# Kernel optimization log

Hardware: AMD Instinct MI355X
Metric: run time of the kernel (lower is better)

Reference implementation:

```python
import jax, jax.numpy as jnp
import numpy as np

S, B, D, H, A = 256, 1024, 64, 128, 8  # seq_len, buffer, state_size, hidden, action_size


def _init(key, shape, fan_in):
    bound = 1.0 / np.sqrt(fan_in)
    return jax.random.uniform(key, shape, jnp.float32, -bound, bound)


def setup_inputs() -> dict:
    key = jax.random.key(0)
    ks = jax.random.split(key, 24)
    inp = {"state": jax.random.normal(ks[0], (S, B, D), jnp.float32)}
    # actor / critic MLPs (Linear(D,H) + ReLU + Linear(H,H) + ReLU)
    inp["aw1"] = _init(ks[1], (H, D), D); inp["ab1"] = _init(ks[2], (H,), D)
    inp["aw2"] = _init(ks[3], (H, H), H); inp["ab2"] = _init(ks[4], (H,), H)
    inp["cw1"] = _init(ks[5], (H, D), D); inp["cb1"] = _init(ks[6], (H,), D)
    inp["cw2"] = _init(ks[7], (H, H), H); inp["cb2"] = _init(ks[8], (H,), H)
    # LSTMs (PyTorch layout: W_ih [4H,H], W_hh [4H,H], gate order i,f,g,o)
    inp["a_wih"] = _init(ks[9], (4 * H, H), H); inp["a_whh"] = _init(ks[10], (4 * H, H), H)
    inp["a_bih"] = _init(ks[11], (4 * H,), H); inp["a_bhh"] = _init(ks[12], (4 * H,), H)
    inp["c_wih"] = _init(ks[13], (4 * H, H), H); inp["c_whh"] = _init(ks[14], (4 * H, H), H)
    inp["c_bih"] = _init(ks[15], (4 * H,), H); inp["c_bhh"] = _init(ks[16], (4 * H,), H)
    # heads
    inp["mw"] = _init(ks[17], (A, H), H); inp["mb"] = _init(ks[18], (A,), H)
    inp["lw"] = _init(ks[19], (A, H), H); inp["lb"] = _init(ks[20], (A,), H)
    inp["vw"] = _init(ks[21], (1, H), H); inp["vb"] = _init(ks[22], (1,), H)
    return inp


def _mlp(x, w1, b1, w2, b2):
    h = jax.nn.relu(jnp.einsum('sbd,hd->sbh', x, w1) + b1)
    return jax.nn.relu(jnp.einsum('sbh,gh->sbg', h, w2) + b2)


def _lstm_zero_state(x, w_ih, b_ih, b_hh):
    # Each timestep runs with fresh zero (h, c): the recurrent term vanishes,
    # so the whole sequence is one batched GEMM + gating (W_hh unused).
    gates = jnp.einsum('sbh,gh->sbg', x, w_ih) + b_ih + b_hh  # [S,B,4H]
    i, f, g, o = jnp.split(gates, 4, axis=-1)
    c = jax.nn.sigmoid(i) * jnp.tanh(g)  # f * c_prev = 0
    return jax.nn.sigmoid(o) * jnp.tanh(c)


def reference(state, aw1, ab1, aw2, ab2, cw1, cb1, cw2, cb2,
              a_wih, a_whh, a_bih, a_bhh, c_wih, c_whh, c_bih, c_bhh,
              mw, mb, lw, lb, vw, vb):
    actor_h = _lstm_zero_state(_mlp(state, aw1, ab1, aw2, ab2), a_wih, a_bih, a_bhh)
    critic_h = _lstm_zero_state(_mlp(state, cw1, cb1, cw2, cb2), c_wih, c_bih, c_bhh)
    mean = jnp.einsum('sbh,ah->sba', actor_h, mw) + mb
    std = jnp.exp(jnp.einsum('sbh,ah->sba', actor_h, lw) + lb)
    value = jnp.einsum('sbh,vh->sbv', critic_h, vw) + vb
    return (mean, std, value)
```

## Files before the change

### kernel.cpp

```cpp
#include <hip/hip_runtime.h>


#define NROWS (256 * 1024)
#define HID 128
#define ACTD 8

#define W1_OFF 0
#define W2_OFF 16384
#define WI_OFF 49152
#define WG_OFF 81920
#define WO_OFF 114688
#define PSTR 147456
#define HEAD_OFF (2 * PSTR)
#define GB_OFF (HEAD_OFF + 8192)

#define NEG_L (-1.4426950408889634f)
#define TWO_L (2.8853900817779268f)

typedef __attribute__((ext_vector_type(8))) short s16x8;
typedef __attribute__((ext_vector_type(4))) float fx4;
typedef __attribute__((ext_vector_type(2))) float fx2;
typedef __attribute__((ext_vector_type(2))) unsigned int u32x2;
typedef __attribute__((ext_vector_type(4))) unsigned int u32x4;

__device__ __forceinline__ unsigned int cvtpk(float lo, float hi) {
  unsigned int r;
  asm("v_cvt_pk_bf16_f32 %0, %1, %2" : "=v"(r) : "v"(lo), "v"(hi));
  return r;
}
__device__ __forceinline__ float ex2(float x) {
  return __builtin_amdgcn_exp2f(x);
}
__device__ __forceinline__ float frcp(float x) {
  return __builtin_amdgcn_rcpf(x);
}
__device__ __forceinline__ fx2 mk2(float a, float b) {
  fx2 v;
  v[0] = a;
  v[1] = b;
  return v;
}

__device__ __forceinline__ s16x8 frag_ld(const unsigned short* base, int row,
                                         int kbyte, int rowsh) {
  int byte = (row << rowsh) + (kbyte ^ ((row & 7) << 4));
  return *(const s16x8*)((const char*)base + byte);
}

struct wpair {
  s16x8 w0, w1;
};
template <int KC>
__device__ __forceinline__ wpair wload(const char* __restrict__ wimg, int wv,
                                       int kc, int woff) {
  wpair p;
  p.w0 = *(const s16x8*)(wimg + (((wv * 2 + 0) * KC + kc) << 10) + woff);
  p.w1 = *(const s16x8*)(wimg + (((wv * 2 + 1) * KC + kc) << 10) + woff);
  return p;
}

template <int ASH>
__device__ __forceinline__ void gemm_kc(const wpair& p,
                                        const unsigned short* at, int kbyte,
                                        int l15, fx4 acc[4][2]) {
#pragma unroll
  for (int jt = 0; jt < 4; ++jt) {
    s16x8 a = frag_ld(at, jt * 16 + l15, kbyte, ASH);
    acc[jt][0] = __builtin_amdgcn_mfma_f32_16x16x32_bf16(p.w0, a, acc[jt][0], 0, 0, 0);
    acc[jt][1] = __builtin_amdgcn_mfma_f32_16x16x32_bf16(p.w1, a, acc[jt][1], 0, 0, 0);
  }
}

__device__ __forceinline__ void zacc(fx4 acc[4][2]) {
#pragma unroll
  for (int j = 0; j < 4; ++j)
#pragma unroll
    for (int i = 0; i < 2; ++i) acc[j][i] = fx4{0.f, 0.f, 0.f, 0.f};
}
__device__ __forceinline__ void bacc(fx4 acc[4][2], const float* __restrict__ b,
                                     int fb, int g4) {
#pragma unroll
  for (int it = 0; it < 2; ++it) {
    fx4 bv = *(const fx4*)(b + fb + it * 16 + g4);
#pragma unroll
    for (int jt = 0; jt < 4; ++jt) acc[jt][it] = bv;
  }
}

__device__ __forceinline__ void epi_relu(fx4 acc[4][2], unsigned short* obuf,
                                         int fb, int lane) {
  const int g4 = (lane >> 4) << 2;
  const int l15 = lane & 15;
  char* ob = (char*)obuf;
#pragma unroll
  for (int it = 0; it < 2; ++it) {
    int n0 = fb + it * 16 + g4;
#pragma unroll
    for (int jt = 0; jt < 4; ++jt) {
      fx4 v = acc[jt][it];
#pragma unroll
      for (int r = 0; r < 4; ++r) v[r] = fmaxf(v[r], 0.0f);
      u32x2 u;
      u[0] = cvtpk(v[0], v[1]);
      u[1] = cvtpk(v[2], v[3]);
      int m = jt * 16 + l15;
      *(u32x2*)(ob + (m << 8) + ((n0 * 2) ^ ((m & 7) << 4))) = u;
    }
  }
}

__global__ void prep_weights(const float* __restrict__ aw1,
                             const float* __restrict__ aw2,
                             const float* __restrict__ awih,
                             const float* __restrict__ cw1,
                             const float* __restrict__ cw2,
                             const float* __restrict__ cwih,
                             const float* __restrict__ mw,
                             const float* __restrict__ lw,
                             const float* __restrict__ vw,
                             const float* __restrict__ abih,
                             const float* __restrict__ abhh,
                             const float* __restrict__ cbih,
                             const float* __restrict__ cbhh,
                             char* __restrict__ ws) {
  int y = blockIdx.y;
  int idx = blockIdx.x * 256 + threadIdx.x;
  if (y >= 12) {
    if (idx < 384) {
      float* dst = (float*)(ws + GB_OFF + (size_t)(y - 12) * 1536);
      const float* b0 = (y == 12) ? abih : cbih;
      const float* b1 = (y == 12) ? abhh : cbhh;
      int sect = idx >> 7, f = idx & 127;
      int srow = (sect == 0) ? f : (sect == 1) ? 256 + f : 384 + f;
      float scale = (sect == 1) ? TWO_L : NEG_L;
      dst[idx] = scale * (b0[srow] + b1[srow]);
    }
    return;
  }
  if (y >= 10) {
    if (idx >= 256) return;
    int row = idx >> 4, c16 = idx & 15, kc = c16 >> 2, ks = c16 & 3;
    fx4 v0 = {0.f, 0.f, 0.f, 0.f}, v1 = v0;
    if (y == 10) {
      const float* src = (row < 8) ? (mw + (size_t)row * HID + c16 * 8)
                                   : (lw + (size_t)(row - 8) * HID + c16 * 8);
      v0 = ((const fx4*)src)[0];
      v1 = ((const fx4*)src)[1];
    } else if (row == 0) {
      const float* src = vw + c16 * 8;
      v0 = ((const fx4*)src)[0];
      v1 = ((const fx4*)src)[1];
    }
    u32x4 u;
    u[0] = cvtpk(v0[0], v0[1]);
    u[1] = cvtpk(v0[2], v0[3]);
    u[2] = cvtpk(v1[0], v1[1]);
    u[3] = cvtpk(v1[2], v1[3]);
    int dst = ((kc * 4 + ks) * 16 + row) * 16;
    *(u32x4*)(ws + HEAD_OFF + (size_t)(y - 10) * 4096 + dst) = u;
    return;
  }
  const float* src;
  int nch, ksh, KC, off;
  switch (y) {
    case 0:  src = aw1;              nch = 1024; ksh = 3; KC = 2; off = W1_OFF;        break;
    case 1:  src = aw2;              nch = 2048; ksh = 4; KC = 4; off = W2_OFF;        break;
    case 2:  src = awih;             nch = 2048; ksh = 4; KC = 4; off = WI_OFF;        break;
    case 3:  src = awih + 256 * HID; nch = 2048; ksh = 4; KC = 4; off = WG_OFF;        break;
    case 4:  src = awih + 384 * HID; nch = 2048; ksh = 4; KC = 4; off = WO_OFF;        break;
    case 5:  src = cw1;              nch = 1024; ksh = 3; KC = 2; off = PSTR + W1_OFF; break;
    case 6:  src = cw2;              nch = 2048; ksh = 4; KC = 4; off = PSTR + W2_OFF; break;
    case 7:  src = cwih;             nch = 2048; ksh = 4; KC = 4; off = PSTR + WI_OFF; break;
    case 8:  src = cwih + 256 * HID; nch = 2048; ksh = 4; KC = 4; off = PSTR + WG_OFF; break;
    default: src = cwih + 384 * HID; nch = 2048; ksh = 4; KC = 4; off = PSTR + WO_OFF; break;
  }
  if (idx >= nch) return;
  int row = idx >> ksh;
  int c16 = idx & ((1 << ksh) - 1);
  int b2 = row >> 4, r = row & 15, kc = c16 >> 2, ks = c16 & 3;
  const fx4* gp = (const fx4*)(src + (size_t)idx * 8);
  fx4 v0 = gp[0], v1 = gp[1];
  u32x4 u;
  u[0] = cvtpk(v0[0], v0[1]);
  u[1] = cvtpk(v0[2], v0[3]);
  u[2] = cvtpk(v1[0], v1[1]);
  u[3] = cvtpk(v1[2], v1[3]);
  int dst = (((b2 * KC + kc) * 4 + ks) * 16 + r) * 16;
  *(u32x4*)(ws + off + dst) = u;
}

__global__ __launch_bounds__(256, 3) void fused_ac(
    const float* __restrict__ state, const float* __restrict__ ab1,
    const float* __restrict__ ab2, const float* __restrict__ cb1,
    const float* __restrict__ cb2, const float* __restrict__ mb,
    const float* __restrict__ lb, const float* __restrict__ vb,
    const char* __restrict__ ws, float* __restrict__ outp) {
  __shared__ __align__(16) unsigned short abuf[8192];
  __shared__ __align__(16) unsigned short hbuf[8192];

  const int tid = threadIdx.x;
  const int lane = tid & 63;
  const int wv = tid >> 6;
  const int l15 = lane & 15;
  const int g4 = (lane >> 4) << 2;
  const int kb0 = (lane >> 4) << 4;
  const int woff = ((lane >> 4) << 8) + (l15 << 4);
  const int fb = wv << 5;
  const int path = blockIdx.x >> 12;
  const int rbase = (blockIdx.x & 4095) << 6;

  const char* wsp = ws + (size_t)path * PSTR;
  const float* b1 = path ? cb1 : ab1;
  const float* b2 = path ? cb2 : ab2;
  const float* gb = (const float*)(ws + GB_OFF + (size_t)path * 1536);
  const char* himg = ws + HEAD_OFF + (size_t)path * 4096;

  float* meanp = outp;
  float* stdp = outp + (size_t)NROWS * ACTD;
  float* valp = outp + (size_t)NROWS * ACTD * 2;

  wpair w1a = wload<2>(wsp + W1_OFF, wv, 0, woff);
  wpair w1b = wload<2>(wsp + W1_OFF, wv, 1, woff);

  {
    const float* xg = state + (size_t)rbase * 64;
    char* ab = (char*)abuf;
#pragma unroll
    for (int i = 0; i < 2; ++i) {
      int idx = tid + i * 256;
      int r = idx >> 3, c = idx & 7;
      const fx4* gp = (const fx4*)(xg + idx * 8);
      fx4 v0 = gp[0], v1 = gp[1];
      u32x4 u;
      u[0] = cvtpk(v0[0], v0[1]);
      u[1] = cvtpk(v0[2], v0[3]);
      u[2] = cvtpk(v1[0], v1[1]);
      u[3] = cvtpk(v1[2], v1[3]);
      *(u32x4*)(ab + r * 128 + ((c << 4) ^ ((r & 7) << 4))) = u;
    }
  }
  __syncthreads();

  fx4 acc[4][2];
  bacc(acc, b1, fb, g4);
  __builtin_amdgcn_s_setprio(1);
  gemm_kc<7>(w1a, abuf, 0 + kb0, l15, acc);
  gemm_kc<7>(w1b, abuf, 64 + kb0, l15, acc);
  __builtin_amdgcn_s_setprio(0);
  wpair w2a = wload<4>(wsp + W2_OFF, wv, 0, woff);
  wpair w2b = wload<4>(wsp + W2_OFF, wv, 1, woff);
  epi_relu(acc, hbuf, fb, lane);
  __syncthreads();

  bacc(acc, b2, fb, g4);
  __builtin_amdgcn_s_setprio(1);
  gemm_kc<8>(w2a, hbuf, 0 + kb0, l15, acc);
  gemm_kc<8>(w2b, hbuf, 64 + kb0, l15, acc);
  {
    wpair p = wload<4>(wsp + W2_OFF, wv, 2, woff);
    gemm_kc<8>(p, hbuf, 128 + kb0, l15, acc);
  }
  {
    wpair p = wload<4>(wsp + W2_OFF, wv, 3, woff);
    gemm_kc<8>(p, hbuf, 192 + kb0, l15, acc);
  }
  __builtin_amdgcn_s_setprio(0);
  wpair pi0 = wload<4>(wsp + WI_OFF, wv, 0, woff);
  wpair pg0 = wload<4>(wsp + WG_OFF, wv, 0, woff);
  wpair po0 = wload<4>(wsp + WO_OFF, wv, 0, woff);
  epi_relu(acc, abuf, fb, lane);
  __syncthreads();

  fx4 ai[4][2], ag[4][2], ao[4][2];
  zacc(ai);
  zacc(ag);
  zacc(ao);
  __builtin_amdgcn_s_setprio(1);
#pragma unroll
  for (int kc = 0; kc < 4; ++kc) {
    wpair pi = (kc == 0) ? pi0 : wload<4>(wsp + WI_OFF, wv, kc, woff);
    wpair pg = (kc == 0) ? pg0 : wload<4>(wsp + WG_OFF, wv, kc, woff);
    wpair po = (kc == 0) ? po0 : wload<4>(wsp + WO_OFF, wv, kc, woff);
    int kbyte = kc * 64 + kb0;
#pragma unroll
    for (int jt = 0; jt < 4; ++jt) {
      s16x8 a = frag_ld(abuf, jt * 16 + l15, kbyte, 8);
      ai[jt][0] = __builtin_amdgcn_mfma_f32_16x16x32_bf16(pi.w0, a, ai[jt][0], 0, 0, 0);
      ai[jt][1] = __builtin_amdgcn_mfma_f32_16x16x32_bf16(pi.w1, a, ai[jt][1], 0, 0, 0);
      ag[jt][0] = __builtin_amdgcn_mfma_f32_16x16x32_bf16(pg.w0, a, ag[jt][0], 0, 0, 0);
      ag[jt][1] = __builtin_amdgcn_mfma_f32_16x16x32_bf16(pg.w1, a, ag[jt][1], 0, 0, 0);
      ao[jt][0] = __builtin_amdgcn_mfma_f32_16x16x32_bf16(po.w0, a, ao[jt][0], 0, 0, 0);
      ao[jt][1] = __builtin_amdgcn_mfma_f32_16x16x32_bf16(po.w1, a, ao[jt][1], 0, 0, 0);
    }
  }
  __builtin_amdgcn_s_setprio(0);
  s16x8 hw0 = *(const s16x8*)(himg + (0 << 10) + woff);
  s16x8 hw1 = *(const s16x8*)(himg + (1 << 10) + woff);
  s16x8 hw2 = *(const s16x8*)(himg + (2 << 10) + woff);
  s16x8 hw3 = *(const s16x8*)(himg + (3 << 10) + woff);

  {
    char* ob = (char*)hbuf;
#pragma unroll
    for (int it = 0; it < 2; ++it) {
      fx4 pvi = *(const fx4*)(gb + fb + it * 16 + g4);
      fx4 pvg = *(const fx4*)(gb + 128 + fb + it * 16 + g4);
      fx4 pvo = *(const fx4*)(gb + 256 + fb + it * 16 + g4);
      int n0 = fb + it * 16 + g4;
#pragma unroll
      for (int jt = 0; jt < 4; ++jt) {
        u32x2 u;
#pragma unroll
        for (int p = 0; p < 2; ++p) {
          const int r0 = 2 * p, r1 = 2 * p + 1;
          fx2 vi = mk2(ai[jt][it][r0], ai[jt][it][r1]);
          fx2 vg = mk2(ag[jt][it][r0], ag[jt][it][r1]);
          fx2 vo = mk2(ao[jt][it][r0], ao[jt][it][r1]);
          fx2 ti = vi * NEG_L + mk2(pvi[r0], pvi[r1]);
          fx2 tg = vg * TWO_L + mk2(pvg[r0], pvg[r1]);
          fx2 to = vo * NEG_L + mk2(pvo[r0], pvo[r1]);
          fx2 Ei = mk2(ex2(ti[0]), ex2(ti[1]));
          fx2 Eg = mk2(ex2(tg[0]), ex2(tg[1]));
          fx2 Eo = mk2(ex2(to[0]), ex2(to[1]));
          fx2 d1 = (Eg + 1.0f) * (Ei + 1.0f);
          fx2 r1v = mk2(frcp(d1[0]), frcp(d1[1]));
          fx2 c = (Eg - 1.0f) * r1v;
          fx2 ea = c * TWO_L;
          fx2 Ec = mk2(ex2(ea[0]), ex2(ea[1]));
          fx2 d2 = (Ec + 1.0f) * (Eo + 1.0f);
          fx2 r2v = mk2(frcp(d2[0]), frcp(d2[1]));
          fx2 h2 = (Ec - 1.0f) * r2v;
          u[p] = cvtpk(h2[0], h2[1]);
        }
        int m = jt * 16 + l15;
        *(u32x2*)(ob + (m << 8) + ((n0 * 2) ^ ((m & 7) << 4))) = u;
      }
    }
  }
  __syncthreads();

  fx4 ha = fx4{0.f, 0.f, 0.f, 0.f};
  __builtin_amdgcn_s_setprio(1);
  ha = __builtin_amdgcn_mfma_f32_16x16x32_bf16(
      hw0, frag_ld(hbuf, (wv << 4) + l15, 0 + kb0, 8), ha, 0, 0, 0);
  ha = __builtin_amdgcn_mfma_f32_16x16x32_bf16(
      hw1, frag_ld(hbuf, (wv << 4) + l15, 64 + kb0, 8), ha, 0, 0, 0);
  ha = __builtin_amdgcn_mfma_f32_16x16x32_bf16(
      hw2, frag_ld(hbuf, (wv << 4) + l15, 128 + kb0, 8), ha, 0, 0, 0);
  ha = __builtin_amdgcn_mfma_f32_16x16x32_bf16(
      hw3, frag_ld(hbuf, (wv << 4) + l15, 192 + kb0, 8), ha, 0, 0, 0);
  __builtin_amdgcn_s_setprio(0);

  int m = rbase + (wv << 4) + l15;
  if (path == 0) {
    if (g4 < 8) {
      fx4 v = ha + *(const fx4*)(mb + g4);
      *(fx4*)(meanp + (size_t)m * ACTD + g4) = v;
    } else {
      fx4 v;
#pragma unroll
      for (int r = 0; r < 4; ++r) v[r] = __expf(ha[r] + lb[g4 - 8 + r]);
      *(fx4*)(stdp + (size_t)m * ACTD + (g4 - 8)) = v;
    }
  } else if (g4 == 0) {
    valp[m] = ha[0] + vb[0];
  }
}

extern "C" void kernel_launch(void* const* d_in, const int* in_sizes, int n_in,
                              void* d_out, int out_size, void* d_ws,
                              size_t ws_size, hipStream_t stream) {
  (void)in_sizes; (void)n_in; (void)ws_size; (void)out_size;
  const float* state = (const float*)d_in[0];
  const float* aw1 = (const float*)d_in[1];
  const float* ab1 = (const float*)d_in[2];
  const float* aw2 = (const float*)d_in[3];
  const float* ab2 = (const float*)d_in[4];
  const float* cw1 = (const float*)d_in[5];
  const float* cb1 = (const float*)d_in[6];
  const float* cw2 = (const float*)d_in[7];
  const float* cb2 = (const float*)d_in[8];
  const float* awih = (const float*)d_in[9];
  const float* abih = (const float*)d_in[11];
  const float* abhh = (const float*)d_in[12];
  const float* cwih = (const float*)d_in[13];
  const float* cbih = (const float*)d_in[15];
  const float* cbhh = (const float*)d_in[16];
  const float* mw = (const float*)d_in[17];
  const float* mb = (const float*)d_in[18];
  const float* lw = (const float*)d_in[19];
  const float* lb = (const float*)d_in[20];
  const float* vw = (const float*)d_in[21];
  const float* vb = (const float*)d_in[22];
  char* ws = (char*)d_ws;

  prep_weights<<<dim3(8, 14), 256, 0, stream>>>(
      aw1, aw2, awih, cw1, cw2, cwih, mw, lw, vw, abih, abhh, cbih, cbhh, ws);
  fused_ac<<<8192, 256, 0, stream>>>(state, ab1, ab2, cb1, cb2, mb, lb, vb, ws,
                                     (float*)d_out);
}
```

Measured before the change: 116.5 us.

## Split LSTM gate GEMM into row quarters to cut registers, raise occupancy

The LSTM gate GEMM now runs in four 16-row passes, each followed by its gating epilogue. Live accumulators drop from 24 fx4 to 6 fx4, and launch bounds go from 3 to 4 blocks per SIMD to raise occupancy. In exchange, the W_i/W_g/W_o weight fragments are reloaded from global memory in every pass, four times as many weight loads. The head weight loads also move to after the gating loop.

```diff
diff --git a/kernel.cpp b/kernel.cpp
--- a/kernel.cpp
+++ b/kernel.cpp
@@ -71,12 +71,6 @@
   }
 }
 
-__device__ __forceinline__ void zacc(fx4 acc[4][2]) {
-#pragma unroll
-  for (int j = 0; j < 4; ++j)
-#pragma unroll
-    for (int i = 0; i < 2; ++i) acc[j][i] = fx4{0.f, 0.f, 0.f, 0.f};
-}
 __device__ __forceinline__ void bacc(fx4 acc[4][2], const float* __restrict__ b,
                                      int fb, int g4) {
 #pragma unroll
@@ -189,7 +183,7 @@
   *(u32x4*)(ws + off + dst) = u;
 }
 
-__global__ __launch_bounds__(256, 3) void fused_ac(
+__global__ __launch_bounds__(256, 4) void fused_ac(
     const float* __restrict__ state, const float* __restrict__ ab1,
     const float* __restrict__ ab2, const float* __restrict__ cb1,
     const float* __restrict__ cb2, const float* __restrict__ mb,
@@ -265,41 +259,34 @@
     gemm_kc<8>(p, hbuf, 192 + kb0, l15, acc);
   }
   __builtin_amdgcn_s_setprio(0);
-  wpair pi0 = wload<4>(wsp + WI_OFF, wv, 0, woff);
-  wpair pg0 = wload<4>(wsp + WG_OFF, wv, 0, woff);
-  wpair po0 = wload<4>(wsp + WO_OFF, wv, 0, woff);
   epi_relu(acc, abuf, fb, lane);
   __syncthreads();
 
-  fx4 ai[4][2], ag[4][2], ao[4][2];
-  zacc(ai);
-  zacc(ag);
-  zacc(ao);
-  __builtin_amdgcn_s_setprio(1);
-#pragma unroll
-  for (int kc = 0; kc < 4; ++kc) {
-    wpair pi = (kc == 0) ? pi0 : wload<4>(wsp + WI_OFF, wv, kc, woff);
-    wpair pg = (kc == 0) ? pg0 : wload<4>(wsp + WG_OFF, wv, kc, woff);
-    wpair po = (kc == 0) ? po0 : wload<4>(wsp + WO_OFF, wv, kc, woff);
-    int kbyte = kc * 64 + kb0;
-#pragma unroll
-    for (int jt = 0; jt < 4; ++jt) {
-      s16x8 a = frag_ld(abuf, jt * 16 + l15, kbyte, 8);
-      ai[jt][0] = __builtin_amdgcn_mfma_f32_16x16x32_bf16(pi.w0, a, ai[jt][0], 0, 0, 0);
-      ai[jt][1] = __builtin_amdgcn_mfma_f32_16x16x32_bf16(pi.w1, a, ai[jt][1], 0, 0, 0);
-      ag[jt][0] = __builtin_amdgcn_mfma_f32_16x16x32_bf16(pg.w0, a, ag[jt][0], 0, 0, 0);
-      ag[jt][1] = __builtin_amdgcn_mfma_f32_16x16x32_bf16(pg.w1, a, ag[jt][1], 0, 0, 0);
-      ao[jt][0] = __builtin_amdgcn_mfma_f32_16x16x32_bf16(po.w0, a, ao[jt][0], 0, 0, 0);
-      ao[jt][1] = __builtin_amdgcn_mfma_f32_16x16x32_bf16(po.w1, a, ao[jt][1], 0, 0, 0);
-    }
-  }
-  __builtin_amdgcn_s_setprio(0);
-  s16x8 hw0 = *(const s16x8*)(himg + (0 << 10) + woff);
-  s16x8 hw1 = *(const s16x8*)(himg + (1 << 10) + woff);
-  s16x8 hw2 = *(const s16x8*)(himg + (2 << 10) + woff);
-  s16x8 hw3 = *(const s16x8*)(himg + (3 << 10) + woff);
-
-  {
+#pragma unroll
+  for (int q = 0; q < 4; ++q) {
+    const int ro = q << 4;
+    fx4 ai[2], ag[2], ao[2];
+#pragma unroll
+    for (int it = 0; it < 2; ++it) {
+      ai[it] = fx4{0.f, 0.f, 0.f, 0.f};
+      ag[it] = fx4{0.f, 0.f, 0.f, 0.f};
+      ao[it] = fx4{0.f, 0.f, 0.f, 0.f};
+    }
+    __builtin_amdgcn_s_setprio(1);
+#pragma unroll
+    for (int kc = 0; kc < 4; ++kc) {
+      wpair pi = wload<4>(wsp + WI_OFF, wv, kc, woff);
+      wpair pg = wload<4>(wsp + WG_OFF, wv, kc, woff);
+      wpair po = wload<4>(wsp + WO_OFF, wv, kc, woff);
+      s16x8 a = frag_ld(abuf, ro + l15, kc * 64 + kb0, 8);
+      ai[0] = __builtin_amdgcn_mfma_f32_16x16x32_bf16(pi.w0, a, ai[0], 0, 0, 0);
+      ai[1] = __builtin_amdgcn_mfma_f32_16x16x32_bf16(pi.w1, a, ai[1], 0, 0, 0);
+      ag[0] = __builtin_amdgcn_mfma_f32_16x16x32_bf16(pg.w0, a, ag[0], 0, 0, 0);
+      ag[1] = __builtin_amdgcn_mfma_f32_16x16x32_bf16(pg.w1, a, ag[1], 0, 0, 0);
+      ao[0] = __builtin_amdgcn_mfma_f32_16x16x32_bf16(po.w0, a, ao[0], 0, 0, 0);
+      ao[1] = __builtin_amdgcn_mfma_f32_16x16x32_bf16(po.w1, a, ao[1], 0, 0, 0);
+    }
+    __builtin_amdgcn_s_setprio(0);
     char* ob = (char*)hbuf;
 #pragma unroll
     for (int it = 0; it < 2; ++it) {
@@ -307,36 +294,37 @@
       fx4 pvg = *(const fx4*)(gb + 128 + fb + it * 16 + g4);
       fx4 pvo = *(const fx4*)(gb + 256 + fb + it * 16 + g4);
       int n0 = fb + it * 16 + g4;
-#pragma unroll
-      for (int jt = 0; jt < 4; ++jt) {
-        u32x2 u;
-#pragma unroll
-        for (int p = 0; p < 2; ++p) {
-          const int r0 = 2 * p, r1 = 2 * p + 1;
-          fx2 vi = mk2(ai[jt][it][r0], ai[jt][it][r1]);
-          fx2 vg = mk2(ag[jt][it][r0], ag[jt][it][r1]);
-          fx2 vo = mk2(ao[jt][it][r0], ao[jt][it][r1]);
-          fx2 ti = vi * NEG_L + mk2(pvi[r0], pvi[r1]);
-          fx2 tg = vg * TWO_L + mk2(pvg[r0], pvg[r1]);
-          fx2 to = vo * NEG_L + mk2(pvo[r0], pvo[r1]);
-          fx2 Ei = mk2(ex2(ti[0]), ex2(ti[1]));
-          fx2 Eg = mk2(ex2(tg[0]), ex2(tg[1]));
-          fx2 Eo = mk2(ex2(to[0]), ex2(to[1]));
-          fx2 d1 = (Eg + 1.0f) * (Ei + 1.0f);
-          fx2 r1v = mk2(frcp(d1[0]), frcp(d1[1]));
-          fx2 c = (Eg - 1.0f) * r1v;
-          fx2 ea = c * TWO_L;
-          fx2 Ec = mk2(ex2(ea[0]), ex2(ea[1]));
-          fx2 d2 = (Ec + 1.0f) * (Eo + 1.0f);
-          fx2 r2v = mk2(frcp(d2[0]), frcp(d2[1]));
-          fx2 h2 = (Ec - 1.0f) * r2v;
-          u[p] = cvtpk(h2[0], h2[1]);
-        }
-        int m = jt * 16 + l15;
-        *(u32x2*)(ob + (m << 8) + ((n0 * 2) ^ ((m & 7) << 4))) = u;
+      u32x2 u;
+#pragma unroll
+      for (int p = 0; p < 2; ++p) {
+        const int r0 = 2 * p, r1 = 2 * p + 1;
+        fx2 vi = mk2(ai[it][r0], ai[it][r1]);
+        fx2 vg = mk2(ag[it][r0], ag[it][r1]);
+        fx2 vo = mk2(ao[it][r0], ao[it][r1]);
+        fx2 ti = vi * NEG_L + mk2(pvi[r0], pvi[r1]);
+        fx2 tg = vg * TWO_L + mk2(pvg[r0], pvg[r1]);
+        fx2 to = vo * NEG_L + mk2(pvo[r0], pvo[r1]);
+        fx2 Ei = mk2(ex2(ti[0]), ex2(ti[1]));
+        fx2 Eg = mk2(ex2(tg[0]), ex2(tg[1]));
+        fx2 Eo = mk2(ex2(to[0]), ex2(to[1]));
+        fx2 d1 = (Eg + 1.0f) * (Ei + 1.0f);
+        fx2 r1v = mk2(frcp(d1[0]), frcp(d1[1]));
+        fx2 c = (Eg - 1.0f) * r1v;
+        fx2 ea = c * TWO_L;
+        fx2 Ec = mk2(ex2(ea[0]), ex2(ea[1]));
+        fx2 d2 = (Ec + 1.0f) * (Eo + 1.0f);
+        fx2 r2v = mk2(frcp(d2[0]), frcp(d2[1]));
+        fx2 h2 = (Ec - 1.0f) * r2v;
+        u[p] = cvtpk(h2[0], h2[1]);
       }
-    }
-  }
+      int m = ro + l15;
+      *(u32x2*)(ob + (m << 8) + ((n0 * 2) ^ ((m & 7) << 4))) = u;
+    }
+  }
+  s16x8 hw0 = *(const s16x8*)(himg + (0 << 10) + woff);
+  s16x8 hw1 = *(const s16x8*)(himg + (1 << 10) + woff);
+  s16x8 hw2 = *(const s16x8*)(himg + (2 << 10) + woff);
+  s16x8 hw3 = *(const s16x8*)(himg + (3 << 10) + woff);
   __syncthreads();
 
   fx4 ha = fx4{0.f, 0.f, 0.f, 0.f};
```

Result: slower. 158.5 us (+36.1%).
